# Kernel optimization log

Hardware: AMD Instinct MI355X
Metric: run time of the kernel (lower is better)

Reference implementation:

```python
import jax, jax.numpy as jnp
import numpy as np

NL = 64      # layers
NOBS = 400   # observed (velocity, period) pairs
NC = 3000    # trial phase velocities in Clist
DAMP = 1.0


def _var(p, q, ra, rb, wvno, xka, xkb, dpth):
    # surf96 'var': layer eigenfunction products, with c<v / c==v / c>v branches
    ra_s = jnp.where(ra > 0, ra, 1.0)
    rb_s = jnp.where(rb > 0, rb, 1.0)
    # P-wave branch
    sinp = jnp.sin(p)
    facp = jnp.where(p < 16.0, jnp.exp(-2.0 * p), 0.0)
    sinp_e = (1.0 - facp) * 0.5
    ltp = wvno < xka
    eqp = wvno == xka
    pex = jnp.where(ltp | eqp, 0.0, p)
    cosp = jnp.where(ltp, jnp.cos(p), jnp.where(eqp, 1.0, (1.0 + facp) * 0.5))
    w = jnp.where(ltp, sinp / ra_s, jnp.where(eqp, dpth, sinp_e / ra_s))
    x = jnp.where(ltp, -ra * sinp, jnp.where(eqp, 0.0, ra * sinp_e))
    # S-wave branch
    sinq = jnp.sin(q)
    facq = jnp.where(q < 16.0, jnp.exp(-2.0 * q), 0.0)
    sinq_e = (1.0 - facq) * 0.5
    lts = wvno < xkb
    eqs = wvno == xkb
    sex = jnp.where(lts | eqs, 0.0, q)
    cosq = jnp.where(lts, jnp.cos(q), jnp.where(eqs, 1.0, (1.0 + facq) * 0.5))
    y = jnp.where(lts, sinq / rb_s, jnp.where(eqs, dpth, sinq_e / rb_s))
    z = jnp.where(lts, -rb * sinq, jnp.where(eqs, 0.0, rb * sinq_e))

    exa = pex + sex
    a0 = jnp.where(exa < 60.0, jnp.exp(-exa), 0.0)
    return a0, cosp * cosq, cosp * y, cosp * z, cosq * w, cosq * x, x * y, x * z, w * y, w * z


def _dltar4(cvel, tper, d, a, b, rho):
    """Rayleigh dispersion determinant (Dunkin) for a flat batch of (c, T) pairs."""
    omega = jnp.maximum(2.0 * jnp.pi / tper, 1.0e-4)
    wvno = omega / cvel
    wvno2 = wvno * wvno

    def rs(v):
        xk = omega / v
        return xk, jnp.sqrt((wvno + xk) * jnp.abs(wvno - xk))

    # bottom half-space compound E vector
    xka, ra = rs(a[-1])
    xkb, rb = rs(b[-1])
    gammk = 2.0 * (b[-1] / omega) ** 2
    gam = gammk * wvno2
    gamm1 = gam - 1.0
    r = rho[-1]
    e = jnp.stack([
        r * r * (gamm1 * gamm1 - gam * gammk * ra * rb),
        -r * ra,
        r * (gamm1 - gammk * ra * rb),
        r * rb,
        wvno2 - ra * rb,
    ], axis=-1)  # [N,5]

    def step(e, lay):
        dm, am, bm, rm = lay
        xka, ra = rs(am)
        xkb, rb = rs(bm)
        gammk = 2.0 * (bm / omega) ** 2
        gam = gammk * wvno2
        p = ra * dm
        q = rb * dm
        a0, cpcq, cpy, cpz, cqw, cqx, xy, xz, wy, wz = _var(p, q, ra, rb, wvno, xka, xkb, dm)
        gamm1 = gam - 1.0
        twgm1 = gam + gamm1
        gmgmk = gam * gammk
        gmgm1 = gam * gamm1
        gm1sq = gamm1 * gamm1
        rho2 = rm * rm
        a0pq = a0 - cpcq
        t2 = -2.0 * wvno2
        # Dunkin 5x5 compound matrix (surf96 dnka)
        c00 = cpcq - 2.0 * gmgm1 * a0pq - gmgmk * xz - wvno2 * gm1sq * wy
        c01 = (wvno2 * cpy - cqx) / rm
        c02 = -(twgm1 * a0pq + gammk * xz + wvno2 * gamm1 * wy) / rm
        c03 = (cpz - wvno2 * cqw) / rm
        c04 = -(2.0 * wvno2 * a0pq + xz + wvno2 * wvno2 * wy) / rho2
        c10 = (gmgmk * cpz - gm1sq * cqw) * rm
        c11 = cpcq
        c12 = gammk * cpz - gamm1 * cqw
        c13 = -wz
        c14 = c03
        c30 = (gm1sq * cpy - gmgmk * cqx) * rm
        c31 = -xy
        c32 = gamm1 * cpy - gammk * cqx
        c33 = cpcq
        c34 = c01
        c40 = -(2.0 * gmgmk * gm1sq * a0pq + gmgmk * gmgmk * xz + gm1sq * gm1sq * wy) * rho2
        c41 = c30
        c42 = -(gmgm1 * twgm1 * a0pq + gam * gammk * gammk * xz + gamm1 * gm1sq * wy) * rm
        c43 = c10
        c44 = c00
        c20 = t2 * c42
        c21 = t2 * c32
        c22 = a0 + 2.0 * (cpcq - c00)
        c23 = t2 * c12
        c24 = t2 * c02
        ca = jnp.stack([
            jnp.stack([c00, c01, c02, c03, c04], axis=-1),
            jnp.stack([c10, c11, c12, c13, c14], axis=-1),
            jnp.stack([c20, c21, c22, c23, c24], axis=-1),
            jnp.stack([c30, c31, c32, c33, c34], axis=-1),
            jnp.stack([c40, c41, c42, c43, c44], axis=-1),
        ], axis=-2)  # [N,5,5]
        ee = jnp.einsum('nj,nji->ni', e, ca)
        nrm = jnp.max(jnp.abs(ee), axis=-1, keepdims=True)
        nrm = jnp.where(nrm < 1e-30, 1.0, nrm)  # surf96 normc
        return ee / nrm, None

    layers = (d[:-1], a[:-1], b[:-1], rho[:-1])
    e, _ = jax.lax.scan(step, e, layers, reverse=True)  # m = nL-2 ... 0 (llw = -1)
    return e[:, 0]


def _brocher(b):
    a = 0.9409 + 2.0947 * b - 0.8206 * b ** 2 + 0.2683 * b ** 3 - 0.0251 * b ** 4
    rho = 1.6612 * a - 0.4721 * a ** 2 + 0.0671 * a ** 3 - 0.0043 * a ** 4 + 0.000106 * a ** 5
    return a, rho


def _laplacian(n, dtype):
    L = 2.0 * jnp.eye(n, dtype=dtype) - jnp.eye(n, k=1, dtype=dtype) - jnp.eye(n, k=-1, dtype=dtype)
    return L.at[0, 0].set(1.0).at[n - 1, n - 1].set(1.0)


def _forward(vlist, tlist, d, b, Clist):
    a, rho = _brocher(b)  # initial_method='Brocher'
    e00 = _dltar4(vlist, tlist, d, a, b, rho)  # [N]
    # normalization grid: no_grad in original -> stop_gradient on all inputs
    sg = jax.lax.stop_gradient
    nC, nT = Clist.shape[0], tlist.shape[0]
    cgrid = jnp.repeat(Clist, nT)
    tgrid = jnp.tile(tlist, nC)
    det = _dltar4(sg(cgrid), sg(tgrid), sg(d), sg(a), sg(b), sg(rho)).reshape(nC, nT)
    rng = det.max(axis=0) - det.min(axis=0)  # [nT]
    e00 = e00 / rng
    # compress='exp' (torch: 0.1 ** abs(e00) - 1; normalized det branch is unused downstream)
    e00 = jnp.power(jnp.asarray(0.1, e00.dtype), jnp.abs(e00)) - 1.0
    e00_all = jnp.sum(jnp.abs(e00)) / e00.shape[0]
    L = _laplacian(b.shape[0], b.dtype)
    m_norm = DAMP * (L @ b) / b.shape[0]
    return e00_all + jnp.sum(jnp.abs(m_norm))


def setup_inputs() -> dict:
    key = jax.random.key(0)
    k1, k2 = jax.random.split(key)
    tlist = 0.5 + 19.5 * jax.random.uniform(k1, (NOBS,), dtype=jnp.float32)  # periods (s)
    vlist = 1.0 + 3.0 * jax.random.uniform(k2, (NOBS,), dtype=jnp.float32)   # phase velocities (km/s)
    d = jnp.full((NL,), 0.5, dtype=jnp.float32)                              # thicknesses (km)
    b = jnp.linspace(1.0, 4.5, NL, dtype=jnp.float32)                        # Vs profile (km/s)
    Clist = jnp.linspace(1.0, 4.0, NC, dtype=jnp.float32)                    # trial velocities
    return {"vlist": vlist, "tlist": tlist, "d": d, "b": b, "Clist": Clist}


def reference(vlist, tlist, d, b, Clist):
    return _forward(vlist, tlist, d, b, Clist)
```

## Files before the change

kernel.cpp:

```cpp
#include <hip/hip_runtime.h>
#include <math.h>
#include <float.h>

#define NL      64
#define NOBS    400
#define NC      3000
#define HALF_NC 1500
#define NCHUNK  3
#define TWO_PI_F   6.2831853071795864769f
#define INV_2PI_F  0.15915494309189535f
#define LOG2E_F    1.4426950408889634f
#define LOG2_0P1  -3.3219280948873623f

typedef float fx2 __attribute__((ext_vector_type(2)));

__device__ __forceinline__ float hsin(float x)  { return __builtin_amdgcn_sinf(x); }
__device__ __forceinline__ float hcos(float x)  { return __builtin_amdgcn_cosf(x); }
__device__ __forceinline__ float hexp2(float x) { return __builtin_amdgcn_exp2f(x); }
__device__ __forceinline__ float hrcp(float x)  { return __builtin_amdgcn_rcpf(x); }
__device__ __forceinline__ float hrsq(float x)  { return __builtin_amdgcn_rsqf(x); }

__device__ __forceinline__ fx2 v_rsq (fx2 v) { fx2 r; r.x = hrsq(v.x);  r.y = hrsq(v.y);  return r; }
__device__ __forceinline__ fx2 v_rcp (fx2 v) { fx2 r; r.x = hrcp(v.x);  r.y = hrcp(v.y);  return r; }
__device__ __forceinline__ fx2 v_sin (fx2 v) { fx2 r; r.x = hsin(v.x);  r.y = hsin(v.y);  return r; }
__device__ __forceinline__ fx2 v_cos (fx2 v) { fx2 r; r.x = hcos(v.x);  r.y = hcos(v.y);  return r; }
__device__ __forceinline__ fx2 v_exp2(fx2 v) { fx2 r; r.x = hexp2(v.x); r.y = hexp2(v.y); return r; }
__device__ __forceinline__ fx2 v_abs (fx2 v) { fx2 r; r.x = fabsf(v.x); r.y = fabsf(v.y); return r; }
__device__ __forceinline__ fx2 v_max (fx2 a, fx2 b) { fx2 r; r.x = fmaxf(a.x, b.x); r.y = fmaxf(a.y, b.y); return r; }

__device__ __forceinline__ unsigned enc(float f) {
    unsigned u = __float_as_uint(f);
    return (u & 0x80000000u) ? ~u : (u | 0x80000000u);
}
__device__ __forceinline__ float dec(unsigned k) {
    unsigned u = (k & 0x80000000u) ? (k & 0x7fffffffu) : ~k;
    return __uint_as_float(u);
}

__global__ void prep_kernel(const float* __restrict__ b, float* __restrict__ a_out,
                            float* __restrict__ rho_out,
                            unsigned* __restrict__ maxenc, unsigned* __restrict__ minenc) {
    int i = threadIdx.x;
    if (i < NL) {
        float bb = b[i];
        float b2 = bb * bb, b3 = b2 * bb, b4 = b3 * bb;
        float a = 0.9409f + 2.0947f * bb - 0.8206f * b2 + 0.2683f * b3 - 0.0251f * b4;
        float a2 = a * a, a3 = a2 * a, a4 = a3 * a, a5 = a4 * a;
        float rho = 1.6612f * a - 0.4721f * a2 + 0.0671f * a3 - 0.0043f * a4 + 0.000106f * a5;
        a_out[i] = a;
        rho_out[i] = rho;
    }
    for (int j = i; j < NOBS; j += 256) {
        maxenc[j] = 0u;
        minenc[j] = 0xFFFFFFFFu;
    }
}


struct SideVals { float cosv, wv, xv, gv; };

__device__ __forceinline__ SideVals side_mixed(float ra, bool lt, float dms,
                                               float dmeh, float ir) {
    float s = hsin(ra * dms);
    float c = hcos(ra * dms);
    float g = hexp2(ra * dmeh);
    float f = g * g;
    float se = 0.5f - 0.5f * f;
    SideVals r;
    r.cosv = lt ? c : (0.5f + 0.5f * f);
    r.wv = (lt ? s : se) * ir;
    r.xv = ra * (lt ? -s : se);
    r.gv = lt ? 1.0f : g;
    return r;
}

template <bool NORM>
__device__ __forceinline__ void layer_step(
    fx2& f0, fx2& f1, fx2& f2, fx2& f3, fx2& f4,
    const float* __restrict__ P, fx2 wvno2, fx2 t2) {

    float xka2 = P[0], xkb2 = P[1], gammk = P[2];
    float dms = P[3], dmeh = P[4];
    float rr = P[5], rr2 = P[6];

    f1 *= rr; f2 *= rr; f3 *= rr; f4 *= rr2;

    fx2 ra2 = wvno2 - xka2;
    fx2 rb2 = wvno2 - xkb2;
    fx2 ra2a = v_max(v_abs(ra2), (fx2)1e-30f);
    fx2 rb2a = v_max(v_abs(rb2), (fx2)1e-30f);
    fx2 ira = v_rsq(ra2a);
    fx2 irb = v_rsq(rb2a);
    fx2 ra = ra2a * ira;
    fx2 rb = rb2a * irb;
    fx2 gam = gammk * wvno2;

    bool px = ra2.x < 0.0f, py = ra2.y < 0.0f;
    bool sx = rb2.x < 0.0f, sy = rb2.y < 0.0f;

    bool allP_prop = __all(px && py);
    bool allP_evan = __all(!(px || py));
    bool allS_prop = __all(sx && sy);
    bool allS_evan = __all(!(sx || sy));

    fx2 cosp, w, x, gp;
    if (allP_prop) {
        fx2 arg = ra * dms;
        fx2 s = v_sin(arg);
        cosp = v_cos(arg);
        w = s * ira;
        x = -(ra * s);
        gp = (fx2)1.0f;
    } else if (allP_evan) {
        fx2 g = v_exp2(ra * dmeh);
        fx2 f = g * g;
        fx2 se = 0.5f - 0.5f * f;
        cosp = 0.5f + 0.5f * f;
        w = se * ira;
        x = ra * se;
        gp = g;
    } else {
        SideVals vx = side_mixed(ra.x, px, dms, dmeh, ira.x);
        SideVals vy = side_mixed(ra.y, py, dms, dmeh, ira.y);
        cosp.x = vx.cosv; w.x = vx.wv; x.x = vx.xv; gp.x = vx.gv;
        cosp.y = vy.cosv; w.y = vy.wv; x.y = vy.xv; gp.y = vy.gv;
    }

    fx2 cosq, y, z, gq;
    if (allS_prop) {
        fx2 arg = rb * dms;
        fx2 s = v_sin(arg);
        cosq = v_cos(arg);
        y = s * irb;
        z = -(rb * s);
        gq = (fx2)1.0f;
    } else if (allS_evan) {
        fx2 g = v_exp2(rb * dmeh);
        fx2 f = g * g;
        fx2 se = 0.5f - 0.5f * f;
        cosq = 0.5f + 0.5f * f;
        y = se * irb;
        z = rb * se;
        gq = g;
    } else {
        SideVals vx = side_mixed(rb.x, sx, dms, dmeh, irb.x);
        SideVals vy = side_mixed(rb.y, sy, dms, dmeh, irb.y);
        cosq.x = vx.cosv; y.x = vx.wv; z.x = vx.xv; gq.x = vx.gv;
        cosq.y = vy.cosv; y.y = vy.wv; z.y = vy.xv; gq.y = vy.gv;
    }

    fx2 a0;
    if (allP_prop && allS_prop) {
        a0 = (fx2)1.0f;
    } else {
        a0 = gp * gq;
    }

    fx2 cpcq = cosp * cosq;
    fx2 cpy = cosp * y, cpz = cosp * z;
    fx2 cqw = cosq * w, cqx = cosq * x;
    fx2 xy = x * y, xz = x * z, wy = w * y, wz = w * z;

    fx2 gamm1 = gam - 1.0f;
    fx2 twgm1 = gam + gamm1;
    fx2 gmgmk = gam * gammk;
    fx2 gmgm1 = gam * gamm1;
    fx2 gm1sq = gamm1 * gamm1;

    fx2 a0pq  = a0 - cpcq;
    fx2 a0pq2 = a0pq + a0pq;
    fx2 nwy   = wvno2 * wy;
    fx2 gw    = gm1sq * wy;

    fx2 c00  = cpcq - gmgm1 * a0pq2 - gmgmk * xz - gm1sq * nwy;
    fx2 c01  = wvno2 * cpy - cqx;
    fx2 nc02 = twgm1 * a0pq + gammk * xz + gamm1 * nwy;
    fx2 c03  = cpz - wvno2 * cqw;
    fx2 nc04 = wvno2 * a0pq2 + xz + wvno2 * nwy;
    fx2 c10  = gmgmk * cpz - gm1sq * cqw;
    fx2 c12  = gammk * cpz - gamm1 * cqw;
    fx2 c30  = gm1sq * cpy - gmgmk * cqx;
    fx2 c32  = gamm1 * cpy - gammk * cqx;
    fx2 t40  = gm1sq * a0pq2 + gmgmk * xz;
    fx2 nc40 = gmgmk * t40 + gm1sq * gw;
    fx2 th   = gmgm1 * twgm1;
    fx2 nc42 = th * a0pq + (gmgmk * gammk) * xz + gamm1 * gw;
    fx2 c22  = a0 + 2.0f * (cpcq - c00);

    fx2 e2t = f2 * t2;

    fx2 ee0 =  f0 * c00  + f1 * c10  - e2t * nc42 + f3 * c30  - f4 * nc40;
    fx2 ee1 =  f0 * c01  + f1 * cpcq + e2t * c32  - f3 * xy   + f4 * c30;
    fx2 ee2 = -f0 * nc02 + f1 * c12  + f2 * c22   + f3 * c32  - f4 * nc42;
    fx2 ee3 =  f0 * c03  - f1 * wz   + e2t * c12  + f3 * cpcq + f4 * c10;
    fx2 ee4 = -f0 * nc04 + f1 * c03  - e2t * nc02 + f3 * c01  + f4 * c00;

    if (NORM) {
        fx2 nv = v_max(v_max(v_abs(ee0), v_abs(ee1)), v_max(v_abs(ee2), v_abs(ee3)));
        nv = v_max(nv, v_abs(ee4));
        nv = v_max(nv, (fx2)1e-30f);
        fx2 inv;
        inv.x = __uint_as_float(0x7f000000u - (__float_as_uint(nv.x) & 0x7f800000u));
        inv.y = __uint_as_float(0x7f000000u - (__float_as_uint(nv.y) & 0x7f800000u));
        f0 = ee0 * inv; f1 = ee1 * inv; f2 = ee2 * inv; f3 = ee3 * inv; f4 = ee4 * inv;
    } else {
        f0 = ee0; f1 = ee1; f2 = ee2; f3 = ee3; f4 = ee4;
    }
}

__device__ fx2 det_eval(fx2 cvel, float omega, const float* __restrict__ Lf, float ir0) {
    fx2 wvno  = omega * v_rcp(cvel);
    fx2 wvno2 = wvno * wvno;
    fx2 t2    = -2.0f * wvno2;

    const float* P = &Lf[(NL - 1) * 8];
    fx2 ra2a = v_max(v_abs(wvno2 - P[0]), (fx2)1e-30f);
    fx2 rb2a = v_max(v_abs(wvno2 - P[1]), (fx2)1e-30f);
    fx2 ra = ra2a * v_rsq(ra2a);
    fx2 rb = rb2a * v_rsq(rb2a);
    float gammk = P[2];
    fx2 gam = gammk * wvno2;
    fx2 gamm1 = gam - 1.0f;
    fx2 rarb = ra * rb;

    fx2 f0 = gamm1 * gamm1 - gam * gammk * rarb;
    fx2 f1 = -ra;
    fx2 f2 = gamm1 - gammk * rarb;
    fx2 f3 = rb;
    fx2 f4 = wvno2 - rarb;

    #pragma unroll 1
    for (int m = NL - 2; m >= 5; m -= 3) {
        layer_step<false>(f0, f1, f2, f3, f4, &Lf[m * 8], wvno2, t2);
        layer_step<false>(f0, f1, f2, f3, f4, &Lf[(m - 1) * 8], wvno2, t2);
        layer_step<true >(f0, f1, f2, f3, f4, &Lf[(m - 2) * 8], wvno2, t2);
    }
    layer_step<false>(f0, f1, f2, f3, f4, &Lf[2 * 8], wvno2, t2);
    layer_step<false>(f0, f1, f2, f3, f4, &Lf[1 * 8], wvno2, t2);
    layer_step<false>(f0, f1, f2, f3, f4, &Lf[0 * 8], wvno2, t2);

    fx2 res;
    {
        float m123 = fmaxf(fmaxf(fabsf(f1.x), fabsf(f2.x)), fabsf(f3.x)) * ir0;
        float nrm = fmaxf(fabsf(f0.x), fmaxf(m123, fabsf(f4.x) * (ir0 * ir0)));
        res.x = f0.x * hrcp(nrm);
    }
    {
        float m123 = fmaxf(fmaxf(fabsf(f1.y), fabsf(f2.y)), fabsf(f3.y)) * ir0;
        float nrm = fmaxf(fabsf(f0.y), fmaxf(m123, fabsf(f4.y) * (ir0 * ir0)));
        res.y = f0.y * hrcp(nrm);
    }
    return res;
}

__global__ __launch_bounds__(256, 2) void det_kernel(
    const float* __restrict__ vlist, const float* __restrict__ tlist,
    const float* __restrict__ d, const float* __restrict__ b,
    const float* __restrict__ Clist,
    const float* __restrict__ a_arr, const float* __restrict__ rho_arr,
    unsigned* __restrict__ maxenc, unsigned* __restrict__ minenc,
    float* __restrict__ e00vals) {

    __shared__ float Lf[NL * 8];
    __shared__ float s_ir0;

    int t     = blockIdx.y;
    int chunk = blockIdx.x;
    int tid   = threadIdx.x;

    float omega = fmaxf(TWO_PI_F / tlist[t], 0.0001f);

    if (tid < NL) {
        float am = a_arr[tid];
        float bm = b[tid];
        float dm = d[tid];
        float* P = &Lf[tid * 8];
        float ta = omega / am;
        float tb = omega / bm;
        P[0] = ta * ta;
        P[1] = tb * tb;
        float tt = bm / omega;
        P[2] = 2.0f * tt * tt;
        P[3] = dm * INV_2PI_F;
        P[4] = -LOG2E_F * dm;
        float rr = (tid < NL - 1) ? (rho_arr[tid] / rho_arr[tid + 1]) : 1.0f;
        P[5] = rr;
        P[6] = rr * rr;
        P[7] = 0.0f;
        if (tid == 0) s_ir0 = 1.0f / rho_arr[0];
    }
    __syncthreads();

    float lmax = -FLT_MAX, lmin = FLT_MAX;
    int base = chunk * 512;

    #pragma unroll 1
    for (int r = 0; r < 2; ++r) {
        int idx = base + r * 256 + tid;
        if (idx <= HALF_NC) {
            bool grid_pt = idx < HALF_NC;
            fx2 cv;
            if (grid_pt) {
                cv.x = Clist[2 * idx];
                cv.y = Clist[2 * idx + 1];
            } else {
                float v = vlist[t];
                cv.x = v; cv.y = v;
            }
            fx2 det = det_eval(cv, omega, Lf, s_ir0);
            if (grid_pt) {
                lmax = fmaxf(lmax, fmaxf(det.x, det.y));
                lmin = fminf(lmin, fminf(det.x, det.y));
            } else {
                e00vals[t] = det.x;
            }
        }
    }

    #pragma unroll
    for (int off = 32; off >= 1; off >>= 1) {
        lmax = fmaxf(lmax, __shfl_xor(lmax, off));
        lmin = fminf(lmin, __shfl_xor(lmin, off));
    }
    if ((tid & 63) == 0) {
        atomicMax(&maxenc[t], enc(lmax));
        atomicMin(&minenc[t], enc(lmin));
    }
}

__global__ __launch_bounds__(512) void finalize_kernel(
    const float* __restrict__ b,
    const unsigned* __restrict__ maxenc, const unsigned* __restrict__ minenc,
    const float* __restrict__ e00vals, float* __restrict__ out) {

    int tid = threadIdx.x;
    float acc = 0.0f;

    if (tid < NOBS) {
        float mx = dec(maxenc[tid]);
        float mn = dec(minenc[tid]);
        float rng  = mx - mn;
        float e00  = e00vals[tid] / rng;
        float term = exp2f(LOG2_0P1 * fabsf(e00)) - 1.0f;
        acc = fabsf(term) * (1.0f / (float)NOBS);
    }
    if (tid < NL) {
        float bi = b[tid];
        float lb;
        if (tid == 0)            lb = bi - b[1];
        else if (tid == NL - 1)  lb = bi - b[NL - 2];
        else                     lb = 2.0f * bi - b[tid - 1] - b[tid + 1];
        acc += fabsf(lb * (1.0f / (float)NL));
    }

    __shared__ float s[512];
    s[tid] = acc;
    __syncthreads();
    for (int st = 256; st > 0; st >>= 1) {
        if (tid < st) s[tid] += s[tid + st];
        __syncthreads();
    }
    if (tid == 0) out[0] = s[0];
}

extern "C" void kernel_launch(void* const* d_in, const int* in_sizes, int n_in,
                              void* d_out, int out_size, void* d_ws, size_t ws_size,
                              hipStream_t stream) {
    const float* vlist = (const float*)d_in[0];
    const float* tlist = (const float*)d_in[1];
    const float* d     = (const float*)d_in[2];
    const float* b     = (const float*)d_in[3];
    const float* Clist = (const float*)d_in[4];
    float* out = (float*)d_out;

    float*    ws      = (float*)d_ws;
    float*    a_arr   = ws;
    float*    rho_arr = ws + 64;
    float*    e00v    = ws + 128;
    unsigned* maxenc  = (unsigned*)(ws + 528);
    unsigned* minenc  = (unsigned*)(ws + 928);

    prep_kernel<<<1, 256, 0, stream>>>(b, a_arr, rho_arr, maxenc, minenc);
    det_kernel<<<dim3(NCHUNK, NOBS), 256, 0, stream>>>(vlist, tlist, d, b, Clist,
                                                       a_arr, rho_arr, maxenc, minenc, e00v);
    finalize_kernel<<<1, 512, 0, stream>>>(b, maxenc, minenc, e00v, out);
}
```

Before: 210.8 us.

## Precompute per-period layer tables in separate kernel, read from global memory

Adds a prep2 kernel that builds the per-period layer parameter table (and omega, 1/rho0) in workspace global memory, so det_kernel no longer fills shared memory and syncs at block start. det_kernel now reads the layer table through global memory, with uniform addresses, instead of LDS. det_eval is also marked noinline. This removes per-block setup and the barrier, and may free the LDS. In exchange it adds a kernel launch and global or scalar loads inside the hot layer loop, and the noinline call adds overhead.

```diff
diff --git a/kernel.cpp b/kernel.cpp
--- a/kernel.cpp
+++ b/kernel.cpp
@@ -53,6 +53,33 @@
     for (int j = i; j < NOBS; j += 256) {
         maxenc[j] = 0u;
         minenc[j] = 0xFFFFFFFFu;
+    }
+}
+
+__global__ void prep2_kernel(const float* __restrict__ tlist, const float* __restrict__ d,
+                             const float* __restrict__ b,
+                             const float* __restrict__ a_arr, const float* __restrict__ rho_arr,
+                             float* __restrict__ tabL, float* __restrict__ tab2) {
+    int t = blockIdx.x;
+    int m = threadIdx.x;
+    float omega = fmaxf(TWO_PI_F / tlist[t], 0.0001f);
+    float am = a_arr[m], bm = b[m], dm = d[m];
+    float ta = omega / am;
+    float tb = omega / bm;
+    float tt = bm / omega;
+    float* P = tabL + t * (NL * 8) + m * 8;
+    P[0] = ta * ta;
+    P[1] = tb * tb;
+    P[2] = 2.0f * tt * tt;
+    P[3] = dm * INV_2PI_F;
+    P[4] = -LOG2E_F * dm;
+    float rr = (m < NL - 1) ? (rho_arr[m] / rho_arr[m + 1]) : 1.0f;
+    P[5] = rr;
+    P[6] = rr * rr;
+    P[7] = 0.0f;
+    if (m == 0) {
+        tab2[2 * t]     = omega;
+        tab2[2 * t + 1] = 1.0f / rho_arr[0];
     }
 }
 
@@ -208,12 +235,14 @@
     }
 }
 
-__device__ fx2 det_eval(fx2 cvel, float omega, const float* __restrict__ Lf, float ir0) {
+__device__ __attribute__((noinline)) fx2 det_eval(
+    fx2 cvel, float omega, const float* __restrict__ T, float ir0) {
+
     fx2 wvno  = omega * v_rcp(cvel);
     fx2 wvno2 = wvno * wvno;
     fx2 t2    = -2.0f * wvno2;
 
-    const float* P = &Lf[(NL - 1) * 8];
+    const float* P = &T[(NL - 1) * 8];
     fx2 ra2a = v_max(v_abs(wvno2 - P[0]), (fx2)1e-30f);
     fx2 rb2a = v_max(v_abs(wvno2 - P[1]), (fx2)1e-30f);
     fx2 ra = ra2a * v_rsq(ra2a);
@@ -231,13 +260,13 @@
 
     #pragma unroll 1
     for (int m = NL - 2; m >= 5; m -= 3) {
-        layer_step<false>(f0, f1, f2, f3, f4, &Lf[m * 8], wvno2, t2);
-        layer_step<false>(f0, f1, f2, f3, f4, &Lf[(m - 1) * 8], wvno2, t2);
-        layer_step<true >(f0, f1, f2, f3, f4, &Lf[(m - 2) * 8], wvno2, t2);
-    }
-    layer_step<false>(f0, f1, f2, f3, f4, &Lf[2 * 8], wvno2, t2);
-    layer_step<false>(f0, f1, f2, f3, f4, &Lf[1 * 8], wvno2, t2);
-    layer_step<false>(f0, f1, f2, f3, f4, &Lf[0 * 8], wvno2, t2);
+        layer_step<false>(f0, f1, f2, f3, f4, &T[m * 8], wvno2, t2);
+        layer_step<false>(f0, f1, f2, f3, f4, &T[(m - 1) * 8], wvno2, t2);
+        layer_step<true >(f0, f1, f2, f3, f4, &T[(m - 2) * 8], wvno2, t2);
+    }
+    layer_step<false>(f0, f1, f2, f3, f4, &T[2 * 8], wvno2, t2);
+    layer_step<false>(f0, f1, f2, f3, f4, &T[1 * 8], wvno2, t2);
+    layer_step<false>(f0, f1, f2, f3, f4, &T[0 * 8], wvno2, t2);
 
     fx2 res;
     {
@@ -254,42 +283,18 @@
 }
 
 __global__ __launch_bounds__(256, 2) void det_kernel(
-    const float* __restrict__ vlist, const float* __restrict__ tlist,
-    const float* __restrict__ d, const float* __restrict__ b,
-    const float* __restrict__ Clist,
-    const float* __restrict__ a_arr, const float* __restrict__ rho_arr,
+    const float* __restrict__ vlist, const float* __restrict__ Clist,
+    const float* __restrict__ tabL, const float* __restrict__ tab2,
     unsigned* __restrict__ maxenc, unsigned* __restrict__ minenc,
     float* __restrict__ e00vals) {
-
-    __shared__ float Lf[NL * 8];
-    __shared__ float s_ir0;
 
     int t     = blockIdx.y;
     int chunk = blockIdx.x;
     int tid   = threadIdx.x;
 
-    float omega = fmaxf(TWO_PI_F / tlist[t], 0.0001f);
-
-    if (tid < NL) {
-        float am = a_arr[tid];
-        float bm = b[tid];
-        float dm = d[tid];
-        float* P = &Lf[tid * 8];
-        float ta = omega / am;
-        float tb = omega / bm;
-        P[0] = ta * ta;
-        P[1] = tb * tb;
-        float tt = bm / omega;
-        P[2] = 2.0f * tt * tt;
-        P[3] = dm * INV_2PI_F;
-        P[4] = -LOG2E_F * dm;
-        float rr = (tid < NL - 1) ? (rho_arr[tid] / rho_arr[tid + 1]) : 1.0f;
-        P[5] = rr;
-        P[6] = rr * rr;
-        P[7] = 0.0f;
-        if (tid == 0) s_ir0 = 1.0f / rho_arr[0];
-    }
-    __syncthreads();
+    const float* __restrict__ T = tabL + t * (NL * 8);
+    float omega = tab2[2 * t];
+    float ir0   = tab2[2 * t + 1];
 
     float lmax = -FLT_MAX, lmin = FLT_MAX;
     int base = chunk * 512;
@@ -307,7 +312,7 @@
                 float v = vlist[t];
                 cv.x = v; cv.y = v;
             }
-            fx2 det = det_eval(cv, omega, Lf, s_ir0);
+            fx2 det = det_eval(cv, omega, T, ir0);
             if (grid_pt) {
                 lmax = fmaxf(lmax, fmaxf(det.x, det.y));
                 lmin = fminf(lmin, fminf(det.x, det.y));
@@ -379,9 +384,12 @@
     float*    e00v    = ws + 128;
     unsigned* maxenc  = (unsigned*)(ws + 528);
     unsigned* minenc  = (unsigned*)(ws + 928);
+    float*    tab2    = ws + 1328;
+    float*    tabL    = ws + 2128;
 
     prep_kernel<<<1, 256, 0, stream>>>(b, a_arr, rho_arr, maxenc, minenc);
-    det_kernel<<<dim3(NCHUNK, NOBS), 256, 0, stream>>>(vlist, tlist, d, b, Clist,
-                                                       a_arr, rho_arr, maxenc, minenc, e00v);
+    prep2_kernel<<<NOBS, 64, 0, stream>>>(tlist, d, b, a_arr, rho_arr, tabL, tab2);
+    det_kernel<<<dim3(NCHUNK, NOBS), 256, 0, stream>>>(vlist, Clist, tabL, tab2,
+                                                       maxenc, minenc, e00v);
     finalize_kernel<<<1, 512, 0, stream>>>(b, maxenc, minenc, e00v, out);
 }
```

After: 229.4 us. 8.8% more time.
